# Kernel tuning notes

Hardware: AMD Instinct MI355X
Metric: run time of the kernel (lower is better)

The kernel has to match this reference:

```python
import jax, jax.numpy as jnp
import numpy as np

N = 50000      # nodes
E = 800000     # edges (avg degree 16)
DIN = 256
DOUT = 256
EA = 16        # edge_attr_dim
EH = 32        # edge_mlp_hidden
Z = 0.8        # z_ratio
EPS = 1e-5


def _lin_init(k, fin, fout):
    k1, k2 = jax.random.split(k)
    s = 1.0 / np.sqrt(fin)
    W = jax.random.uniform(k1, (fin, fout), jnp.float32, -s, s)
    b = jax.random.uniform(k2, (fout,), jnp.float32, -s, s)
    return W, b


def setup_inputs() -> dict:
    key = jax.random.key(0)
    ks = jax.random.split(key, 12)
    x = jax.random.normal(ks[0], (N, DIN), dtype=jnp.float32)
    edge_index = jax.random.randint(ks[1], (2, E), 0, N, dtype=jnp.int64)
    edge_weight = jax.random.uniform(ks[2], (E,), dtype=jnp.float32)
    mask = jax.random.bernoulli(ks[3], 0.5, (N, 1))
    edge_attr = jax.random.normal(ks[4], (E, EA), dtype=jnp.float32)
    Wt0, bt0 = _lin_init(ks[5], DIN, DOUT)
    Wt1, bt1 = _lin_init(ks[6], DIN, DOUT)
    Wc0, bc0 = _lin_init(ks[7], DIN + DOUT, DOUT)
    Wc1, bc1 = _lin_init(ks[8], DIN + DOUT, DOUT)
    gn_w = jnp.ones((DOUT,), jnp.float32)
    gn_b = jnp.zeros((DOUT,), jnp.float32)
    gn_alpha = jnp.ones((DOUT,), jnp.float32)  # GraphNorm mean_scale
    Wm1, bm1 = _lin_init(ks[9], EA, EH)
    Wm2, bm2 = _lin_init(ks[10], EH, 1)
    return {
        'x': x, 'edge_index': edge_index, 'edge_weight': edge_weight,
        'mask': mask, 'edge_attr': edge_attr,
        'Wt0': Wt0, 'bt0': bt0, 'Wt1': Wt1, 'bt1': bt1,
        'Wc0': Wc0, 'bc0': bc0, 'Wc1': Wc1, 'bc1': bc1,
        'gn_w': gn_w, 'gn_b': gn_b, 'gn_alpha': gn_alpha,
        'Wm1': Wm1, 'bm1': bm1, 'Wm2': Wm2, 'bm2': bm2,
    }


def _mix(m, a1, a0):
    # torch.where(mask, z*x1 + (1-z)*x0, z*x0 + (1-z)*x1)
    return jnp.where(m, Z * a1 + (1.0 - Z) * a0, Z * a0 + (1.0 - Z) * a1)


def reference(x, edge_index, edge_weight, mask, edge_attr,
              Wt0, bt0, Wt1, bt1, Wc0, bc0, Wc1, bc1,
              gn_w, gn_b, gn_alpha, Wm1, bm1, Wm2, bm2):
    n_node = x.shape[0]
    row, col = edge_index[0], edge_index[1]

    # edge MLP (scalar mode): edge_weight <- softplus(MLP(edge_attr))
    h = jax.nn.relu(edge_attr @ Wm1 + bm1)
    ew = jax.nn.softplus((h @ Wm2 + bm2))[:, 0]  # [E]

    # buildAdj with aggr='mean': row-normalized weights
    deg = jax.ops.segment_sum(ew, row, num_segments=n_node)
    deg = jnp.where(deg < 0.5, deg + 1.0, deg)
    w = ew / deg[row]  # [E]

    # dual-branch transform + masked mix
    x1 = jax.nn.relu(x @ Wt1 + bt1)
    x0 = jax.nn.relu(x @ Wt0 + bt0)
    xm = _mix(mask, x1, x0)  # [N, DOUT]

    # sparse adj @ x : gather at col, scatter-add at row
    agg = jax.ops.segment_sum(w[:, None] * xm[col], row, num_segments=n_node)

    # GraphNorm (single graph): x - alpha*mean, normalize by std
    mean = jnp.mean(agg, axis=0)
    out = agg - gn_alpha * mean
    var = jnp.mean(out * out, axis=0)
    out = gn_w * out * jax.lax.rsqrt(var + EPS) + gn_b

    # dropout inactive in eval mode
    xc = jnp.concatenate([out, x], axis=-1)  # [N, DOUT+DIN]
    c1 = xc @ Wc1 + bc1
    c0 = xc @ Wc0 + bc0
    return _mix(mask, c1, c0)
```

## Files before the change

kernel.cpp:

```cpp
#include <hip/hip_runtime.h>

#define NN 50000
#define NE 800000
#define NNP 50176

typedef __attribute__((ext_vector_type(4))) float f32x4;
typedef __bf16 bf16x8 __attribute__((ext_vector_type(8)));

__device__ __forceinline__ float bfu2f(unsigned short u) {
  return __uint_as_float(((unsigned)u) << 16);
}
__device__ __forceinline__ unsigned short f2bf(float f) {
  unsigned u = __float_as_uint(f);
  u += 0x7fffu + ((u >> 16) & 1u);
  return (unsigned short)(u >> 16);
}

__device__ __forceinline__ void gload16(const void* g, void* l) {
  __builtin_amdgcn_global_load_lds(
      (const __attribute__((address_space(1))) unsigned int*)g,
      (__attribute__((address_space(3))) unsigned int*)l, 16, 0, 0);
}

__global__ __launch_bounds__(256) void transpose_w(
    const float* __restrict__ W, unsigned short* __restrict__ WT, int K, int N) {
  __shared__ unsigned short T[32 * 40];
  const int t = threadIdx.x;
  const int k0 = blockIdx.x * 32, n0 = blockIdx.y * 32;
  const int kk = t >> 3, nn = (t & 7) * 4;
  f32x4 v = *(const f32x4*)(W + (k0 + kk) * N + n0 + nn);
#pragma unroll
  for (int i = 0; i < 4; i++) T[(nn + i) * 40 + kk] = f2bf(v[i]);
  __syncthreads();
  const int nn2 = t >> 3, kk2 = (t & 7) * 4;
  unsigned short o[4];
#pragma unroll
  for (int i = 0; i < 4; i++) o[i] = T[nn2 * 40 + kk2 + i];
  *(uint2*)(WT + (n0 + nn2) * K + k0 + kk2) = *(const uint2*)o;
}

__global__ __launch_bounds__(256) void x2bf_kernel(
    const float* __restrict__ X, unsigned short* __restrict__ xbf) {
  const int gid = blockIdx.x * 256 + threadIdx.x;
  const long base = (long)gid * 8;
  const int row = (int)(base >> 8);
  unsigned short o[8];
  if (row < NN) {
    f32x4 a = *(const f32x4*)(X + base);
    f32x4 b = *(const f32x4*)(X + base + 4);
#pragma unroll
    for (int i = 0; i < 4; i++) { o[i] = f2bf(a[i]); o[4 + i] = f2bf(b[i]); }
  } else {
#pragma unroll
    for (int i = 0; i < 8; i++) o[i] = 0;
  }
  *(uint4*)(xbf + base) = *(const uint4*)o;
}

__global__ __launch_bounds__(256) void count_kernel(
    const int* __restrict__ ei, int* __restrict__ cnt, int* __restrict__ rank) {
  const int e = blockIdx.x * 256 + threadIdx.x;
  if (e >= NE) return;
  rank[e] = atomicAdd(&cnt[ei[e]], 1);
}

__global__ __launch_bounds__(256) void scan1_kernel(const int* __restrict__ cnt,
                                                    int* __restrict__ blockSum) {
  __shared__ int sd[256];
  const int t = threadIdx.x;
  sd[t] = cnt[blockIdx.x * 256 + t];
  __syncthreads();
  for (int off = 128; off > 0; off >>= 1) {
    if (t < off) sd[t] += sd[t + off];
    __syncthreads();
  }
  if (t == 0) blockSum[blockIdx.x] = sd[0];
}

__global__ __launch_bounds__(256) void scan2_kernel(int* __restrict__ blockSum) {
  __shared__ int sd[256];
  const int t = threadIdx.x;
  int v = (t < 196) ? blockSum[t] : 0;
  sd[t] = v;
  __syncthreads();
  for (int off = 1; off < 256; off <<= 1) {
    int y = (t >= off) ? sd[t - off] : 0;
    __syncthreads();
    sd[t] += y;
    __syncthreads();
  }
  int ex = (t == 0) ? 0 : sd[t - 1];
  __syncthreads();
  if (t < 196) blockSum[t] = ex;
}

__global__ __launch_bounds__(256) void scan3_kernel(
    const int* __restrict__ cnt, const int* __restrict__ blockSum,
    int* __restrict__ start) {
  __shared__ int sd[256];
  const int t = threadIdx.x;
  const int row = blockIdx.x * 256 + t;
  const int c = cnt[row];
  sd[t] = c;
  __syncthreads();
  for (int off = 1; off < 256; off <<= 1) {
    int y = (t >= off) ? sd[t - off] : 0;
    __syncthreads();
    sd[t] += y;
    __syncthreads();
  }
  start[row] = blockSum[blockIdx.x] + sd[t] - c;
}

__device__ __forceinline__ void mlp4(float a0, float a1, float a2, float a3,
                                     const f32x4* __restrict__ w,
                                     f32x4& h0, f32x4& h1, f32x4& h2, f32x4& h3,
                                     f32x4& h4, f32x4& h5, f32x4& h6, f32x4& h7) {
  h0 += w[0] * a0;  h1 += w[1] * a0;  h2 += w[2] * a0;  h3 += w[3] * a0;
  h4 += w[4] * a0;  h5 += w[5] * a0;  h6 += w[6] * a0;  h7 += w[7] * a0;
  h0 += w[8] * a1;  h1 += w[9] * a1;  h2 += w[10] * a1; h3 += w[11] * a1;
  h4 += w[12] * a1; h5 += w[13] * a1; h6 += w[14] * a1; h7 += w[15] * a1;
  h0 += w[16] * a2; h1 += w[17] * a2; h2 += w[18] * a2; h3 += w[19] * a2;
  h4 += w[20] * a2; h5 += w[21] * a2; h6 += w[22] * a2; h7 += w[23] * a2;
  h0 += w[24] * a3; h1 += w[25] * a3; h2 += w[26] * a3; h3 += w[27] * a3;
  h4 += w[28] * a3; h5 += w[29] * a3; h6 += w[30] * a3; h7 += w[31] * a3;
}

__device__ __forceinline__ float rdot(f32x4 h, f32x4 w) {
  float s = fmaxf(h[0], 0.0f) * w[0];
  s = fmaf(fmaxf(h[1], 0.0f), w[1], s);
  s = fmaf(fmaxf(h[2], 0.0f), w[2], s);
  s = fmaf(fmaxf(h[3], 0.0f), w[3], s);
  return s;
}

__global__ __launch_bounds__(256) void mlp_fill_kernel(
    const float* __restrict__ ea,
    const float* __restrict__ Wm1, const float* __restrict__ bm1,
    const float* __restrict__ Wm2, const float* __restrict__ bm2,
    const int* __restrict__ ei, const int* __restrict__ start,
    const int* __restrict__ rank, uint2* __restrict__ colw) {
  __shared__ __align__(16) float w1[512];
  __shared__ __align__(16) float b1[32];
  __shared__ __align__(16) float w2[32];
  __shared__ float b2s[1];
  const int t = threadIdx.x;
  w1[t] = Wm1[t];
  w1[t + 256] = Wm1[t + 256];
  if (t < 32) { b1[t] = bm1[t]; w2[t] = Wm2[t]; }
  if (t == 0) b2s[0] = bm2[0];
  __syncthreads();
  const int e = blockIdx.x * 256 + t;
  if (e >= NE) return;
  f32x4 r0 = *(const f32x4*)(ea + e * 16);
  f32x4 r1 = *(const f32x4*)(ea + e * 16 + 4);
  f32x4 r2 = *(const f32x4*)(ea + e * 16 + 8);
  f32x4 r3 = *(const f32x4*)(ea + e * 16 + 12);
  const f32x4* bv = (const f32x4*)b1;
  f32x4 h0 = bv[0], h1 = bv[1], h2 = bv[2], h3 = bv[3];
  f32x4 h4 = bv[4], h5 = bv[5], h6 = bv[6], h7 = bv[7];
  const f32x4* wv = (const f32x4*)w1;
  mlp4(r0[0], r0[1], r0[2], r0[3], wv, h0, h1, h2, h3, h4, h5, h6, h7);
  mlp4(r1[0], r1[1], r1[2], r1[3], wv + 32, h0, h1, h2, h3, h4, h5, h6, h7);
  mlp4(r2[0], r2[1], r2[2], r2[3], wv + 64, h0, h1, h2, h3, h4, h5, h6, h7);
  mlp4(r3[0], r3[1], r3[2], r3[3], wv + 96, h0, h1, h2, h3, h4, h5, h6, h7);
  const f32x4* w2v = (const f32x4*)w2;
  float s = b2s[0];
  s += rdot(h0, w2v[0]) + rdot(h1, w2v[1]) + rdot(h2, w2v[2]) + rdot(h3, w2v[3]);
  s += rdot(h4, w2v[4]) + rdot(h5, w2v[5]) + rdot(h6, w2v[6]) + rdot(h7, w2v[7]);
  const float sp = (s > 0.0f) ? (s + log1pf(expf(-s))) : log1pf(expf(s));
  uint2 p;
  p.x = (unsigned)ei[NE + e];
  p.y = __float_as_uint(sp);
  colw[start[ei[e]] + rank[e]] = p;
}

template <int KTOT, bool SPLIT, bool OUT_BF16>
__global__ __launch_bounds__(256, 3) void gemm_dual(
    const unsigned short* __restrict__ A0, const unsigned short* __restrict__ A1,
    const unsigned short* __restrict__ WT1, const unsigned short* __restrict__ WT0,
    const float* __restrict__ bias1, const float* __restrict__ bias0,
    const int* __restrict__ mask, void* __restrict__ outp) {
  __shared__ __align__(16) unsigned short Al[128 * 64];
  __shared__ __align__(16) unsigned short B1l[64 * 64];
  __shared__ __align__(16) unsigned short B0l[64 * 64];
  const int t = threadIdx.x;
  const int bid = blockIdx.y * gridDim.x + blockIdx.x;
  const int swz = (bid & 7) * 196 + (bid >> 3);
  const int bx = swz & 3, by = swz >> 2;
  const int row0 = by * 128, col0 = bx * 64;
  const int wv = t >> 6, lane = t & 63, m = lane & 15, q = lane >> 4;
  const int wr = wv >> 1, wc = wv & 1;
  const int arow = t >> 3, ach = t & 7;
  f32x4 acc1[4][2], acc0[4][2];
#pragma unroll
  for (int rf = 0; rf < 4; rf++)
#pragma unroll
    for (int nt = 0; nt < 2; nt++) { acc1[rf][nt] = (f32x4)(0.0f); acc0[rf][nt] = (f32x4)(0.0f); }

  for (int k0 = 0; k0 < KTOT; k0 += 64) {
    const unsigned short* Ab;
    int kr;
    if constexpr (SPLIT) {
      if (k0 < 256) { Ab = A0; kr = k0; } else { Ab = A1; kr = k0 - 256; }
    } else { Ab = A0; kr = k0; }
#pragma unroll
    for (int i = 0; i < 4; i++) {
      const int r = arow + i * 32;
      gload16(Ab + (size_t)(row0 + r) * 256 + kr + ((ach ^ (r & 7)) << 3),
              &Al[(i * 256 + t) * 8]);
    }
#pragma unroll
    for (int i = 0; i < 2; i++) {
      const int r = arow + i * 32;
      const int sc = (ach ^ (r & 7)) << 3;
      gload16(WT1 + (size_t)(col0 + r) * KTOT + k0 + sc, &B1l[(i * 256 + t) * 8]);
      gload16(WT0 + (size_t)(col0 + r) * KTOT + k0 + sc, &B0l[(i * 256 + t) * 8]);
    }
    __syncthreads();
#pragma unroll
    for (int kk = 0; kk < 2; kk++) {
      bf16x8 af[4];
#pragma unroll
      for (int rf = 0; rf < 4; rf++) {
        const int r = wr * 64 + rf * 16 + m;
        af[rf] = *(const bf16x8*)&Al[r * 64 + (((kk * 4 + q) ^ (r & 7)) << 3)];
      }
#pragma unroll
      for (int nt = 0; nt < 2; nt++) {
        const int n = wc * 32 + nt * 16 + m;
        const int off = n * 64 + (((kk * 4 + q) ^ (n & 7)) << 3);
        bf16x8 f1 = *(const bf16x8*)&B1l[off];
        bf16x8 f0 = *(const bf16x8*)&B0l[off];
#pragma unroll
        for (int rf = 0; rf < 4; rf++) {
          acc1[rf][nt] = __builtin_amdgcn_mfma_f32_16x16x32_bf16(af[rf], f1, acc1[rf][nt], 0, 0, 0);
          acc0[rf][nt] = __builtin_amdgcn_mfma_f32_16x16x32_bf16(af[rf], f0, acc0[rf][nt], 0, 0, 0);
        }
      }
    }
    __syncthreads();
  }

#pragma unroll
  for (int rf = 0; rf < 4; rf++) {
    const int rbase = row0 + wr * 64 + rf * 16 + q * 4;
    int mk[4];
#pragma unroll
    for (int r = 0; r < 4; r++) mk[r] = (rbase + r < NN) ? mask[rbase + r] : 0;
#pragma unroll
    for (int nt = 0; nt < 2; nt++) {
      const int gc = col0 + wc * 32 + nt * 16 + m;
      const float bb1 = bias1[gc];
      const float bb0 = bias0[gc];
#pragma unroll
      for (int r = 0; r < 4; r++) {
        const int grr = rbase + r;
        if (grr < NN) {
          float v1 = acc1[rf][nt][r] + bb1;
          float v0 = acc0[rf][nt][r] + bb0;
          if constexpr (OUT_BF16) {
            v1 = fmaxf(v1, 0.0f);
            v0 = fmaxf(v0, 0.0f);
            float o = mk[r] ? (0.8f * v1 + 0.2f * v0) : (0.8f * v0 + 0.2f * v1);
            ((unsigned short*)outp)[(size_t)grr * 256 + gc] = f2bf(o);
          } else {
            float o = mk[r] ? (0.8f * v1 + 0.2f * v0) : (0.8f * v0 + 0.2f * v1);
            ((float*)outp)[(size_t)grr * 256 + gc] = o;
          }
        }
      }
    }
  }
}

__global__ __launch_bounds__(256) void aggregate_kernel(
    const int* __restrict__ start, const int* __restrict__ cnt,
    const uint2* __restrict__ colw,
    const unsigned short* __restrict__ xmb, unsigned short* __restrict__ aggb) {
  const int wave = threadIdx.x >> 6, lane = threadIdx.x & 63;
  const int row = blockIdx.x * 4 + wave;
  const int s = start[row];
  const int c = cnt[row];
  const int choff = lane * 4;
  f32x4 acc = (f32x4)(0.0f);
  float dsum = 0.0f;
  int i = 0;
  for (; i + 4 <= c; i += 4) {
    uint2 cw0 = colw[s + i], cw1 = colw[s + i + 1];
    uint2 cw2 = colw[s + i + 2], cw3 = colw[s + i + 3];
    const float w0 = __uint_as_float(cw0.y), w1 = __uint_as_float(cw1.y);
    const float w2 = __uint_as_float(cw2.y), w3 = __uint_as_float(cw3.y);
    uint2 u0 = *(const uint2*)(xmb + (int)cw0.x * 256 + choff);
    uint2 u1 = *(const uint2*)(xmb + (int)cw1.x * 256 + choff);
    uint2 u2 = *(const uint2*)(xmb + (int)cw2.x * 256 + choff);
    uint2 u3 = *(const uint2*)(xmb + (int)cw3.x * 256 + choff);
    dsum += (w0 + w1) + (w2 + w3);
    acc[0] = fmaf(w0, __uint_as_float(u0.x << 16), acc[0]);
    acc[1] = fmaf(w0, __uint_as_float(u0.x & 0xffff0000u), acc[1]);
    acc[2] = fmaf(w0, __uint_as_float(u0.y << 16), acc[2]);
    acc[3] = fmaf(w0, __uint_as_float(u0.y & 0xffff0000u), acc[3]);
    acc[0] = fmaf(w1, __uint_as_float(u1.x << 16), acc[0]);
    acc[1] = fmaf(w1, __uint_as_float(u1.x & 0xffff0000u), acc[1]);
    acc[2] = fmaf(w1, __uint_as_float(u1.y << 16), acc[2]);
    acc[3] = fmaf(w1, __uint_as_float(u1.y & 0xffff0000u), acc[3]);
    acc[0] = fmaf(w2, __uint_as_float(u2.x << 16), acc[0]);
    acc[1] = fmaf(w2, __uint_as_float(u2.x & 0xffff0000u), acc[1]);
    acc[2] = fmaf(w2, __uint_as_float(u2.y << 16), acc[2]);
    acc[3] = fmaf(w2, __uint_as_float(u2.y & 0xffff0000u), acc[3]);
    acc[0] = fmaf(w3, __uint_as_float(u3.x << 16), acc[0]);
    acc[1] = fmaf(w3, __uint_as_float(u3.x & 0xffff0000u), acc[1]);
    acc[2] = fmaf(w3, __uint_as_float(u3.y << 16), acc[2]);
    acc[3] = fmaf(w3, __uint_as_float(u3.y & 0xffff0000u), acc[3]);
  }
  for (; i < c; i++) {
    uint2 cw0 = colw[s + i];
    const float w0 = __uint_as_float(cw0.y);
    uint2 u0 = *(const uint2*)(xmb + (int)cw0.x * 256 + choff);
    dsum += w0;
    acc[0] = fmaf(w0, __uint_as_float(u0.x << 16), acc[0]);
    acc[1] = fmaf(w0, __uint_as_float(u0.x & 0xffff0000u), acc[1]);
    acc[2] = fmaf(w0, __uint_as_float(u0.y << 16), acc[2]);
    acc[3] = fmaf(w0, __uint_as_float(u0.y & 0xffff0000u), acc[3]);
  }
  float d = (dsum < 0.5f) ? dsum + 1.0f : dsum;
  const float inv = 1.0f / d;
  unsigned short o[4];
#pragma unroll
  for (int j = 0; j < 4; j++) o[j] = f2bf(acc[j] * inv);
  *(uint2*)(aggb + row * 256 + choff) = *(const uint2*)o;
}

__global__ __launch_bounds__(256) void stats_kernel(
    const unsigned short* __restrict__ aggb, float* __restrict__ S1, float* __restrict__ S2) {
  const int c = threadIdx.x;
  const int r0 = blockIdx.x * 200;
  float s1 = 0.0f, s2 = 0.0f;
  for (int r = 0; r < 200; r++) {
    float v = bfu2f(aggb[(r0 + r) * 256 + c]);
    s1 += v;
    s2 = fmaf(v, v, s2);
  }
  unsafeAtomicAdd(&S1[c], s1);
  unsafeAtomicAdd(&S2[c], s2);
}

__global__ __launch_bounds__(256) void norm_agg_kernel(
    const unsigned short* __restrict__ aggb,
    const float* __restrict__ S1, const float* __restrict__ S2,
    const float* __restrict__ gw, const float* __restrict__ gb,
    const float* __restrict__ ga, unsigned short* __restrict__ aggn) {
  __shared__ float scL[256];
  __shared__ float shL[256];
  const int t = threadIdx.x;
  {
    const float inv_n = 1.0f / (float)NN;
    float mean = S1[t] * inv_n;
    float ex2 = S2[t] * inv_n;
    float am = ga[t] * mean;
    float var = ex2 - 2.0f * am * mean + am * am;
    float sc = gw[t] * rsqrtf(var + 1e-5f);
    scL[t] = sc;
    shL[t] = gb[t] - sc * am;
  }
  __syncthreads();
  const int gid = blockIdx.x * 256 + t;
  const long base = (long)gid * 8;
  const int row = (int)(base >> 8);
  const int c = (int)(base & 255);
  unsigned short o[8];
  if (row < NN) {
    uint4 u = *(const uint4*)(aggb + base);
    const unsigned short* us = (const unsigned short*)&u;
#pragma unroll
    for (int i = 0; i < 8; i++) o[i] = f2bf(fmaf(scL[c + i], bfu2f(us[i]), shL[c + i]));
  } else {
#pragma unroll
    for (int i = 0; i < 8; i++) o[i] = 0;
  }
  *(uint4*)(aggn + base) = *(const uint4*)o;
}

extern "C" void kernel_launch(void* const* d_in, const int* in_sizes, int n_in,
                              void* d_out, int out_size, void* d_ws, size_t ws_size,
                              hipStream_t stream) {
  (void)in_sizes; (void)n_in; (void)out_size; (void)ws_size;
  const float* x   = (const float*)d_in[0];
  const int*   ei  = (const int*)d_in[1];
  const int*   msk = (const int*)d_in[3];
  const float* ea  = (const float*)d_in[4];
  const float* Wt0 = (const float*)d_in[5];
  const float* bt0 = (const float*)d_in[6];
  const float* Wt1 = (const float*)d_in[7];
  const float* bt1 = (const float*)d_in[8];
  const float* Wc0 = (const float*)d_in[9];
  const float* bc0 = (const float*)d_in[10];
  const float* Wc1 = (const float*)d_in[11];
  const float* bc1 = (const float*)d_in[12];
  const float* gnw = (const float*)d_in[13];
  const float* gnb = (const float*)d_in[14];
  const float* gna = (const float*)d_in[15];
  const float* Wm1 = (const float*)d_in[16];
  const float* bm1 = (const float*)d_in[17];
  const float* Wm2 = (const float*)d_in[18];
  const float* bm2 = (const float*)d_in[19];

  char* ws = (char*)d_ws;
  int* cnt      = (int*)ws;
  int* startA   = (int*)(ws + 200704);
  int* blockSum = (int*)(ws + 401408);
  float* S1     = (float*)(ws + 402432);
  float* S2     = (float*)(ws + 403456);
  unsigned short* WTt1 = (unsigned short*)(ws + 404480);
  unsigned short* WTt0 = (unsigned short*)(ws + 535552);
  unsigned short* WTc1 = (unsigned short*)(ws + 666624);
  unsigned short* WTc0 = (unsigned short*)(ws + 928768);
  int* rankA    = (int*)(ws + 1190912);
  uint2* colw   = (uint2*)(ws + 4390912);
  unsigned short* xmb  = (unsigned short*)(ws + 10790912);
  unsigned short* aggb = (unsigned short*)(ws + 36481024);
  unsigned short* xbf  = (unsigned short*)(ws + 62171136);

  hipMemsetAsync(ws, 0, 404480, stream);

  transpose_w<<<dim3(8, 8), 256, 0, stream>>>(Wt1, WTt1, 256, 256);
  transpose_w<<<dim3(8, 8), 256, 0, stream>>>(Wt0, WTt0, 256, 256);
  transpose_w<<<dim3(16, 8), 256, 0, stream>>>(Wc1, WTc1, 512, 256);
  transpose_w<<<dim3(16, 8), 256, 0, stream>>>(Wc0, WTc0, 512, 256);
  x2bf_kernel<<<6272, 256, 0, stream>>>(x, xbf);

  count_kernel<<<3125, 256, 0, stream>>>(ei, cnt, rankA);
  scan1_kernel<<<196, 256, 0, stream>>>(cnt, blockSum);
  scan2_kernel<<<1, 256, 0, stream>>>(blockSum);
  scan3_kernel<<<196, 256, 0, stream>>>(cnt, blockSum, startA);
  mlp_fill_kernel<<<3125, 256, 0, stream>>>(ea, Wm1, bm1, Wm2, bm2, ei, startA, rankA, colw);

  gemm_dual<256, false, true><<<dim3(4, 392), 256, 0, stream>>>(
      xbf, (const unsigned short*)nullptr, WTt1, WTt0, bt1, bt0, msk, xmb);

  aggregate_kernel<<<12500, 256, 0, stream>>>(startA, cnt, colw, xmb, aggb);
  stats_kernel<<<250, 256, 0, stream>>>(aggb, S1, S2);
  norm_agg_kernel<<<6272, 256, 0, stream>>>(aggb, S1, S2, gnw, gnb, gna, xmb );

  gemm_dual<512, true, false><<<dim3(4, 392), 256, 0, stream>>>(
      xmb , xbf, WTc1, WTc0, bc1, bc0, msk, d_out);
}
```

Baseline: 403.8 us.

## Fuse prep kernels and fold GraphNorm stats into restructured aggregation

Merges the weight transposes, x-to-bf16 conversion and edge counting into one prep launch to cut launch overhead. Restructures aggregation so each half-wave handles alternate edges with 16-byte gathers over 8 channels, combines the halves with a shuffle, and loops each wave over several rows with a persistent-style grid. Folds the column sum and sum-of-squares statistics into the aggregation, using per-block shared reductions and atomics, which removes the separate stats pass over aggb. In exchange there are fewer blocks, and the statistics are now computed from fp32 values instead of bf16-rounded ones, which slightly changes the numerics.

```diff
diff --git a/kernel.cpp b/kernel.cpp
--- a/kernel.cpp
+++ b/kernel.cpp
@@ -22,13 +22,49 @@
       (__attribute__((address_space(3))) unsigned int*)l, 16, 0, 0);
 }
 
-__global__ __launch_bounds__(256) void transpose_w(
-    const float* __restrict__ W, unsigned short* __restrict__ WT, int K, int N) {
+__global__ __launch_bounds__(256) void prep_kernel(
+    const float* __restrict__ X, unsigned short* __restrict__ xbf,
+    const int* __restrict__ ei, int* __restrict__ cnt, int* __restrict__ rank,
+    const float* __restrict__ Wt1, const float* __restrict__ Wt0,
+    const float* __restrict__ Wc1, const float* __restrict__ Wc0,
+    unsigned short* __restrict__ WTt1, unsigned short* __restrict__ WTt0,
+    unsigned short* __restrict__ WTc1, unsigned short* __restrict__ WTc0) {
   __shared__ unsigned short T[32 * 40];
-  const int t = threadIdx.x;
-  const int k0 = blockIdx.x * 32, n0 = blockIdx.y * 32;
+  const int bid = blockIdx.x;
+  const int t = threadIdx.x;
+  if (bid < 3125) {
+    const int e = bid * 256 + t;
+    if (e < NE) rank[e] = atomicAdd(&cnt[ei[e]], 1);
+    return;
+  }
+  if (bid < 3125 + 6272) {
+    const int gid = (bid - 3125) * 256 + t;
+    const long base = (long)gid * 8;
+    const int row = (int)(base >> 8);
+    unsigned short o[8];
+    if (row < NN) {
+      f32x4 a = *(const f32x4*)(X + base);
+      f32x4 b = *(const f32x4*)(X + base + 4);
+#pragma unroll
+      for (int i = 0; i < 4; i++) { o[i] = f2bf(a[i]); o[4 + i] = f2bf(b[i]); }
+    } else {
+#pragma unroll
+      for (int i = 0; i < 8; i++) o[i] = 0;
+    }
+    *(uint4*)(xbf + base) = *(const uint4*)o;
+    return;
+  }
+  int tb = bid - (3125 + 6272);
+  const float* W;
+  unsigned short* WT;
+  int K, kx, ny;
+  if (tb < 64) { W = Wt1; WT = WTt1; K = 256; kx = tb & 7; ny = tb >> 3; }
+  else if (tb < 128) { tb -= 64; W = Wt0; WT = WTt0; K = 256; kx = tb & 7; ny = tb >> 3; }
+  else if (tb < 256) { tb -= 128; W = Wc1; WT = WTc1; K = 512; kx = tb & 15; ny = tb >> 4; }
+  else { tb -= 256; W = Wc0; WT = WTc0; K = 512; kx = tb & 15; ny = tb >> 4; }
+  const int k0 = kx * 32, n0 = ny * 32;
   const int kk = t >> 3, nn = (t & 7) * 4;
-  f32x4 v = *(const f32x4*)(W + (k0 + kk) * N + n0 + nn);
+  f32x4 v = *(const f32x4*)(W + (k0 + kk) * 256 + n0 + nn);
 #pragma unroll
   for (int i = 0; i < 4; i++) T[(nn + i) * 40 + kk] = f2bf(v[i]);
   __syncthreads();
@@ -37,31 +73,6 @@
 #pragma unroll
   for (int i = 0; i < 4; i++) o[i] = T[nn2 * 40 + kk2 + i];
   *(uint2*)(WT + (n0 + nn2) * K + k0 + kk2) = *(const uint2*)o;
-}
-
-__global__ __launch_bounds__(256) void x2bf_kernel(
-    const float* __restrict__ X, unsigned short* __restrict__ xbf) {
-  const int gid = blockIdx.x * 256 + threadIdx.x;
-  const long base = (long)gid * 8;
-  const int row = (int)(base >> 8);
-  unsigned short o[8];
-  if (row < NN) {
-    f32x4 a = *(const f32x4*)(X + base);
-    f32x4 b = *(const f32x4*)(X + base + 4);
-#pragma unroll
-    for (int i = 0; i < 4; i++) { o[i] = f2bf(a[i]); o[4 + i] = f2bf(b[i]); }
-  } else {
-#pragma unroll
-    for (int i = 0; i < 8; i++) o[i] = 0;
-  }
-  *(uint4*)(xbf + base) = *(const uint4*)o;
-}
-
-__global__ __launch_bounds__(256) void count_kernel(
-    const int* __restrict__ ei, int* __restrict__ cnt, int* __restrict__ rank) {
-  const int e = blockIdx.x * 256 + threadIdx.x;
-  if (e >= NE) return;
-  rank[e] = atomicAdd(&cnt[ei[e]], 1);
 }
 
 __global__ __launch_bounds__(256) void scan1_kernel(const int* __restrict__ cnt,
@@ -274,75 +285,102 @@
   }
 }
 
+#define AGG_BLOCKS 1563
+#define AGG_SLOTS (AGG_BLOCKS * 4)
+#define AGG_ITERS 8
+
+#define ACC1(u, cw) do { \
+  const float w_ = __uint_as_float(cw.y); \
+  dsum += w_; \
+  accA[0] = fmaf(w_, __uint_as_float(u.x << 16), accA[0]); \
+  accA[1] = fmaf(w_, __uint_as_float(u.x & 0xffff0000u), accA[1]); \
+  accA[2] = fmaf(w_, __uint_as_float(u.y << 16), accA[2]); \
+  accA[3] = fmaf(w_, __uint_as_float(u.y & 0xffff0000u), accA[3]); \
+  accB[0] = fmaf(w_, __uint_as_float(u.z << 16), accB[0]); \
+  accB[1] = fmaf(w_, __uint_as_float(u.z & 0xffff0000u), accB[1]); \
+  accB[2] = fmaf(w_, __uint_as_float(u.w << 16), accB[2]); \
+  accB[3] = fmaf(w_, __uint_as_float(u.w & 0xffff0000u), accB[3]); \
+} while (0)
+
 __global__ __launch_bounds__(256) void aggregate_kernel(
     const int* __restrict__ start, const int* __restrict__ cnt,
     const uint2* __restrict__ colw,
-    const unsigned short* __restrict__ xmb, unsigned short* __restrict__ aggb) {
+    const unsigned short* __restrict__ xmb, unsigned short* __restrict__ aggb,
+    float* __restrict__ S1, float* __restrict__ S2) {
+  __shared__ float s1L[4][256];
+  __shared__ float s2L[4][256];
   const int wave = threadIdx.x >> 6, lane = threadIdx.x & 63;
-  const int row = blockIdx.x * 4 + wave;
-  const int s = start[row];
-  const int c = cnt[row];
-  const int choff = lane * 4;
-  f32x4 acc = (f32x4)(0.0f);
-  float dsum = 0.0f;
-  int i = 0;
-  for (; i + 4 <= c; i += 4) {
-    uint2 cw0 = colw[s + i], cw1 = colw[s + i + 1];
-    uint2 cw2 = colw[s + i + 2], cw3 = colw[s + i + 3];
-    const float w0 = __uint_as_float(cw0.y), w1 = __uint_as_float(cw1.y);
-    const float w2 = __uint_as_float(cw2.y), w3 = __uint_as_float(cw3.y);
-    uint2 u0 = *(const uint2*)(xmb + (int)cw0.x * 256 + choff);
-    uint2 u1 = *(const uint2*)(xmb + (int)cw1.x * 256 + choff);
-    uint2 u2 = *(const uint2*)(xmb + (int)cw2.x * 256 + choff);
-    uint2 u3 = *(const uint2*)(xmb + (int)cw3.x * 256 + choff);
-    dsum += (w0 + w1) + (w2 + w3);
-    acc[0] = fmaf(w0, __uint_as_float(u0.x << 16), acc[0]);
-    acc[1] = fmaf(w0, __uint_as_float(u0.x & 0xffff0000u), acc[1]);
-    acc[2] = fmaf(w0, __uint_as_float(u0.y << 16), acc[2]);
-    acc[3] = fmaf(w0, __uint_as_float(u0.y & 0xffff0000u), acc[3]);
-    acc[0] = fmaf(w1, __uint_as_float(u1.x << 16), acc[0]);
-    acc[1] = fmaf(w1, __uint_as_float(u1.x & 0xffff0000u), acc[1]);
-    acc[2] = fmaf(w1, __uint_as_float(u1.y << 16), acc[2]);
-    acc[3] = fmaf(w1, __uint_as_float(u1.y & 0xffff0000u), acc[3]);
-    acc[0] = fmaf(w2, __uint_as_float(u2.x << 16), acc[0]);
-    acc[1] = fmaf(w2, __uint_as_float(u2.x & 0xffff0000u), acc[1]);
-    acc[2] = fmaf(w2, __uint_as_float(u2.y << 16), acc[2]);
-    acc[3] = fmaf(w2, __uint_as_float(u2.y & 0xffff0000u), acc[3]);
-    acc[0] = fmaf(w3, __uint_as_float(u3.x << 16), acc[0]);
-    acc[1] = fmaf(w3, __uint_as_float(u3.x & 0xffff0000u), acc[1]);
-    acc[2] = fmaf(w3, __uint_as_float(u3.y << 16), acc[2]);
-    acc[3] = fmaf(w3, __uint_as_float(u3.y & 0xffff0000u), acc[3]);
-  }
-  for (; i < c; i++) {
-    uint2 cw0 = colw[s + i];
-    const float w0 = __uint_as_float(cw0.y);
-    uint2 u0 = *(const uint2*)(xmb + (int)cw0.x * 256 + choff);
-    dsum += w0;
-    acc[0] = fmaf(w0, __uint_as_float(u0.x << 16), acc[0]);
-    acc[1] = fmaf(w0, __uint_as_float(u0.x & 0xffff0000u), acc[1]);
-    acc[2] = fmaf(w0, __uint_as_float(u0.y << 16), acc[2]);
-    acc[3] = fmaf(w0, __uint_as_float(u0.y & 0xffff0000u), acc[3]);
-  }
-  float d = (dsum < 0.5f) ? dsum + 1.0f : dsum;
-  const float inv = 1.0f / d;
-  unsigned short o[4];
-#pragma unroll
-  for (int j = 0; j < 4; j++) o[j] = f2bf(acc[j] * inv);
-  *(uint2*)(aggb + row * 256 + choff) = *(const uint2*)o;
-}
-
-__global__ __launch_bounds__(256) void stats_kernel(
-    const unsigned short* __restrict__ aggb, float* __restrict__ S1, float* __restrict__ S2) {
-  const int c = threadIdx.x;
-  const int r0 = blockIdx.x * 200;
-  float s1 = 0.0f, s2 = 0.0f;
-  for (int r = 0; r < 200; r++) {
-    float v = bfu2f(aggb[(r0 + r) * 256 + c]);
-    s1 += v;
-    s2 = fmaf(v, v, s2);
-  }
-  unsafeAtomicAdd(&S1[c], s1);
-  unsafeAtomicAdd(&S2[c], s2);
+  const int half = lane >> 5, hl = lane & 31;
+  const int ch = hl * 8;
+  const int slot = blockIdx.x * 4 + wave;
+  f32x4 rs1a = (f32x4)(0.0f), rs1b = (f32x4)(0.0f);
+  f32x4 rs2a = (f32x4)(0.0f), rs2b = (f32x4)(0.0f);
+  for (int g = 0; g < AGG_ITERS; g++) {
+    const int row = slot + g * AGG_SLOTS;
+    if (row >= NN) break;
+    const int s = start[row];
+    const int c = cnt[row];
+    f32x4 accA = (f32x4)(0.0f), accB = (f32x4)(0.0f);
+    float dsum = 0.0f;
+    int i = 0;
+    for (; i + 8 <= c; i += 8) {
+      uint2 cw0 = colw[s + i + half];
+      uint2 cw1 = colw[s + i + 2 + half];
+      uint2 cw2 = colw[s + i + 4 + half];
+      uint2 cw3 = colw[s + i + 6 + half];
+      uint4 u0 = *(const uint4*)(xmb + (size_t)cw0.x * 256 + ch);
+      uint4 u1 = *(const uint4*)(xmb + (size_t)cw1.x * 256 + ch);
+      uint4 u2 = *(const uint4*)(xmb + (size_t)cw2.x * 256 + ch);
+      uint4 u3 = *(const uint4*)(xmb + (size_t)cw3.x * 256 + ch);
+      ACC1(u0, cw0);
+      ACC1(u1, cw1);
+      ACC1(u2, cw2);
+      ACC1(u3, cw3);
+    }
+    for (; i + 2 <= c; i += 2) {
+      uint2 cw0 = colw[s + i + half];
+      uint4 u0 = *(const uint4*)(xmb + (size_t)cw0.x * 256 + ch);
+      ACC1(u0, cw0);
+    }
+    if (i < c && half == 0) {
+      uint2 cw0 = colw[s + i];
+      uint4 u0 = *(const uint4*)(xmb + (size_t)cw0.x * 256 + ch);
+      ACC1(u0, cw0);
+    }
+#pragma unroll
+    for (int j = 0; j < 4; j++) {
+      accA[j] += __shfl_xor(accA[j], 32);
+      accB[j] += __shfl_xor(accB[j], 32);
+    }
+    dsum += __shfl_xor(dsum, 32);
+    const float d = (dsum < 0.5f) ? dsum + 1.0f : dsum;
+    const float inv = 1.0f / d;
+    if (half == 0) {
+      unsigned short o[8];
+#pragma unroll
+      for (int j = 0; j < 4; j++) {
+        const float vA = accA[j] * inv;
+        const float vB = accB[j] * inv;
+        o[j] = f2bf(vA);
+        o[4 + j] = f2bf(vB);
+        rs1a[j] += vA; rs2a[j] = fmaf(vA, vA, rs2a[j]);
+        rs1b[j] += vB; rs2b[j] = fmaf(vB, vB, rs2b[j]);
+      }
+      *(uint4*)(aggb + (size_t)row * 256 + ch) = *(const uint4*)o;
+    }
+  }
+  if (half == 0) {
+    *(f32x4*)&s1L[wave][ch] = rs1a;
+    *(f32x4*)&s1L[wave][ch + 4] = rs1b;
+    *(f32x4*)&s2L[wave][ch] = rs2a;
+    *(f32x4*)&s2L[wave][ch + 4] = rs2b;
+  }
+  __syncthreads();
+  const int t = threadIdx.x;
+  const float p1 = s1L[0][t] + s1L[1][t] + s1L[2][t] + s1L[3][t];
+  const float p2 = s2L[0][t] + s2L[1][t] + s2L[2][t] + s2L[3][t];
+  unsafeAtomicAdd(&S1[t], p1);
+  unsafeAtomicAdd(&S2[t], p2);
 }
 
 __global__ __launch_bounds__(256) void norm_agg_kernel(
@@ -423,13 +461,9 @@
 
   hipMemsetAsync(ws, 0, 404480, stream);
 
-  transpose_w<<<dim3(8, 8), 256, 0, stream>>>(Wt1, WTt1, 256, 256);
-  transpose_w<<<dim3(8, 8), 256, 0, stream>>>(Wt0, WTt0, 256, 256);
-  transpose_w<<<dim3(16, 8), 256, 0, stream>>>(Wc1, WTc1, 512, 256);
-  transpose_w<<<dim3(16, 8), 256, 0, stream>>>(Wc0, WTc0, 512, 256);
-  x2bf_kernel<<<6272, 256, 0, stream>>>(x, xbf);
-
-  count_kernel<<<3125, 256, 0, stream>>>(ei, cnt, rankA);
+  prep_kernel<<<9781, 256, 0, stream>>>(x, xbf, ei, cnt, rankA,
+                                        Wt1, Wt0, Wc1, Wc0,
+                                        WTt1, WTt0, WTc1, WTc0);
   scan1_kernel<<<196, 256, 0, stream>>>(cnt, blockSum);
   scan2_kernel<<<1, 256, 0, stream>>>(blockSum);
   scan3_kernel<<<196, 256, 0, stream>>>(cnt, blockSum, startA);
@@ -438,8 +472,7 @@
   gemm_dual<256, false, true><<<dim3(4, 392), 256, 0, stream>>>(
       xbf, (const unsigned short*)nullptr, WTt1, WTt0, bt1, bt0, msk, xmb);
 
-  aggregate_kernel<<<12500, 256, 0, stream>>>(startA, cnt, colw, xmb, aggb);
-  stats_kernel<<<250, 256, 0, stream>>>(aggb, S1, S2);
+  aggregate_kernel<<<AGG_BLOCKS, 256, 0, stream>>>(startA, cnt, colw, xmb, aggb, S1, S2);
   norm_agg_kernel<<<6272, 256, 0, stream>>>(aggb, S1, S2, gnw, gnb, gna, xmb );
 
   gemm_dual<512, true, false><<<dim3(4, 392), 256, 0, stream>>>(
```

After: 421.9 us. 4.5% more time.
